# Kernel optimization log

Hardware: AMD Instinct MI355X
Metric: run time of the kernel (lower is better)

## Reference

```python
import jax, jax.numpy as jnp
import numpy as np

N = 100000      # nodes
E = 1600000     # edges (avg degree 16)
D = 64          # in_dim == hidden_dim
L = 4           # layer_gin
G = 128         # graphs in batch
BN_EPS = 1e-5


def setup_inputs() -> dict:
    key = jax.random.key(0)
    ks = jax.random.split(key, 9)
    x = jax.random.normal(ks[0], (N, D), dtype=jnp.float32)
    edge_index = jax.random.randint(ks[1], (2, E), 0, N, dtype=jnp.int32)
    batch = jnp.sort(jax.random.randint(ks[2], (N,), 0, G, dtype=jnp.int32))
    s = 0.05
    W1 = jax.random.normal(ks[3], (L, D, D), dtype=jnp.float32) * s
    b1 = jax.random.normal(ks[4], (L, D), dtype=jnp.float32) * s
    gamma = jnp.ones((L, D), dtype=jnp.float32)
    beta = jnp.zeros((L, D), dtype=jnp.float32)
    W2 = jax.random.normal(ks[5], (L, D, D), dtype=jnp.float32) * s
    b2 = jax.random.normal(ks[6], (L, D), dtype=jnp.float32) * s
    return dict(x=x, edge_index=edge_index, batch=batch,
                W1=W1, b1=b1, gamma=gamma, beta=beta, W2=W2, b2=b2)


def reference(x, edge_index, batch, W1, b1, gamma, beta, W2, b2):
    n = x.shape[0]
    src, dst = edge_index[0], edge_index[1]  # flow source_to_target
    # in-degree for mean aggregation (clamped to avoid div-by-zero)
    deg = jax.ops.segment_sum(jnp.ones(src.shape, x.dtype), dst, num_segments=n)
    inv_deg = 1.0 / jnp.maximum(deg, 1.0)
    # graph sizes for global mean pool
    gcnt = jax.ops.segment_sum(jnp.ones((n,), x.dtype), batch, num_segments=G)
    inv_gcnt = 1.0 / jnp.maximum(gcnt, 1.0)

    h = x
    node_pool = jnp.zeros((n, W2.shape[-1]), x.dtype)
    g_pool = jnp.zeros((G, W2.shape[-1]), x.dtype)
    for l in range(L):  # small fixed layer count
        # scatter-mean neighbor aggregation: [E,D] gather -> segment_sum
        agg = jax.ops.segment_sum(h[src], dst, num_segments=n) * inv_deg[:, None]
        z = (h + agg) @ W1[l] + b1[l]          # eps=0: (1+eps)*x + mean_j x_j
        mu = z.mean(axis=0)
        var = z.var(axis=0)                     # biased, as torch BatchNorm1d
        z = (z - mu) * jax.lax.rsqrt(var + BN_EPS) * gamma[l] + beta[l]
        h = jax.nn.relu(z) @ W2[l] + b2[l]
        node_pool = node_pool + h
        g_pool = g_pool + jax.ops.segment_sum(h, batch, num_segments=G) * inv_gcnt[:, None]
    return node_pool, g_pool
```

## Files before the change

kernel.cpp:

```cpp
#include <hip/hip_runtime.h>

#define N_NODES 100000
#define N_EDGES 1600000
#define DIM 64
#define NLAYER 4
#define NGRAPH 128
#define BN_EPS 1e-5f
#define NSHARD 16
#define AGG_CHUNK 16
#define NCHUNK (N_NODES / AGG_CHUNK)

typedef unsigned short ushort_t;
typedef unsigned int uint_t;
typedef __attribute__((ext_vector_type(8))) short short8;
typedef __attribute__((ext_vector_type(4))) float f32x4;
typedef __attribute__((ext_vector_type(4))) uint_t uintx4;

__device__ __forceinline__ ushort_t f2bf(float f) {
    uint_t u = __float_as_uint(f);
    uint_t r = (u + 0x7FFFu + ((u >> 16) & 1u)) >> 16;
    return (ushort_t)r;
}
__device__ __forceinline__ float bf2f(ushort_t u) {
    return __uint_as_float((uint_t)u << 16);
}
__device__ __forceinline__ void bf8_to_f32(const uint4 v, float f[8]) {
    f[0] = __uint_as_float(v.x << 16);
    f[1] = __uint_as_float(v.x & 0xFFFF0000u);
    f[2] = __uint_as_float(v.y << 16);
    f[3] = __uint_as_float(v.y & 0xFFFF0000u);
    f[4] = __uint_as_float(v.z << 16);
    f[5] = __uint_as_float(v.z & 0xFFFF0000u);
    f[6] = __uint_as_float(v.w << 16);
    f[7] = __uint_as_float(v.w & 0xFFFF0000u);
}


__global__ void k_hist(const int* __restrict__ ei, int* __restrict__ cntS,
                       int* __restrict__ rank,
                       const float* __restrict__ x, ushort_t* __restrict__ xh) {
    int e = blockIdx.x * blockDim.x + threadIdx.x;
    if (e < N_EDGES) {
        const float4 v = ((const float4*)x)[e];
        int d = ei[N_EDGES + e];
        int s = blockIdx.x & (NSHARD - 1);
        rank[e] = atomicAdd(&cntS[s * N_NODES + d], 1);
        ushort4 u;
        u.x = f2bf(v.x); u.y = f2bf(v.y); u.z = f2bf(v.z); u.w = f2bf(v.w);
        ((ushort4*)xh)[e] = u;
    }
}

__global__ void k_sumscan(int* __restrict__ cntS, int* __restrict__ cnt,
                          int* __restrict__ exc, int* __restrict__ bsums) {
    __shared__ int s[256];
    int i = blockIdx.x * 256 + threadIdx.x;
    int run = 0;
    if (i < N_NODES) {
#pragma unroll
        for (int sh = 0; sh < NSHARD; sh++) {
            int c = cntS[sh * N_NODES + i];
            cntS[sh * N_NODES + i] = run;
            run += c;
        }
        cnt[i] = run;
    }
    s[threadIdx.x] = run;
    __syncthreads();
    for (int off = 1; off < 256; off <<= 1) {
        int t = (threadIdx.x >= off) ? s[threadIdx.x - off] : 0;
        __syncthreads();
        s[threadIdx.x] += t;
        __syncthreads();
    }
    if (i < N_NODES) exc[i] = s[threadIdx.x] - run;
    if (threadIdx.x == 255) bsums[blockIdx.x] = s[255];
}

__global__ void k_scan2(const int* __restrict__ bsums, int* __restrict__ boffs, int nb) {
    __shared__ int s[512];
    int v = ((int)threadIdx.x < nb) ? bsums[threadIdx.x] : 0;
    s[threadIdx.x] = v;
    __syncthreads();
    for (int off = 1; off < 512; off <<= 1) {
        int t = (threadIdx.x >= off) ? s[threadIdx.x - off] : 0;
        __syncthreads();
        s[threadIdx.x] += t;
        __syncthreads();
    }
    if ((int)threadIdx.x < nb) boffs[threadIdx.x] = s[threadIdx.x] - v;
}

__global__ void k_scan3(int* __restrict__ exc, const int* __restrict__ boffs,
                        const int* __restrict__ cnt, const int* __restrict__ batch,
                        float* __restrict__ invdeg, float* __restrict__ invg) {
    int i = blockIdx.x * 256 + threadIdx.x;
    if (i < N_NODES) {
        exc[i] += boffs[blockIdx.x];
        invdeg[i] = 1.0f / (float)max(cnt[i], 1);
    }
    if (i < NGRAPH) {
        int key = i, lo = 0, hi = N_NODES;
        while (lo < hi) { int m = (lo + hi) >> 1; if (batch[m] < key) lo = m + 1; else hi = m; }
        int a = lo;
        key = i + 1; lo = 0; hi = N_NODES;
        while (lo < hi) { int m = (lo + hi) >> 1; if (batch[m] < key) lo = m + 1; else hi = m; }
        invg[i] = 1.0f / (float)max(lo - a, 1);
    }
}

__global__ void k_fill(const int* __restrict__ ei, const int* __restrict__ rowptr,
                       const int* __restrict__ cntS, const int* __restrict__ rank,
                       int* __restrict__ csr) {
    int e = blockIdx.x * blockDim.x + threadIdx.x;
    if (e < N_EDGES) {
        int d = ei[N_EDGES + e];
        int s = blockIdx.x & (NSHARD - 1);
        csr[rowptr[d] + cntS[s * N_NODES + d] + rank[e]] = ei[e];
    }
}

__device__ __forceinline__ void grp8b(const ushort_t* __restrict__ h,
                                      const int* __restrict__ cp,
                                      int e, int deg, int q, int r,
                                      float acc[8]) {
    const int last = deg - 1;
    const int e0 = e + q;
    int i0 = cp[min(e0, last)];
    float m0 = (e0 < deg) ? 1.f : 0.f;
    const uint4 v = *(const uint4*)(h + (size_t)i0 * 64 + r * 8);
    float f[8];
    bf8_to_f32(v, f);
#pragma unroll
    for (int j = 0; j < 8; j++) acc[j] = fmaf(f[j], m0, acc[j]);
}


__global__ __launch_bounds__(256, 8)
void k_passA(const ushort_t* __restrict__ h, const float* __restrict__ W1,
             const float* __restrict__ b1,
             const int* __restrict__ rowptr, const int* __restrict__ cnt,
             const int* __restrict__ csr, const float* __restrict__ invdeg,
             ushort_t* __restrict__ tglob, float* __restrict__ colsum,
             float* __restrict__ colsumsq) {
    __shared__ ushort_t wfrag[512 * 8];
    __shared__ uint_t smt[4][16 * 36];
    __shared__ float red[128];

    const int w = threadIdx.x >> 6;
    const int lane = threadIdx.x & 63;
    const int q = lane >> 3;
    const int r = lane & 7;
    const int wid = __builtin_amdgcn_readfirstlane((blockIdx.x << 2) | w);
    const bool active = wid < NCHUNK;
    const int n0 = (active ? wid : 0) * AGG_CHUNK;

    for (int s = threadIdx.x; s < 512; s += 256) {
        const int hh = s >> 8, c = (s >> 6) & 3, L = s & 63;
        const int kb = hh * 32 + ((L >> 4) * 8);
        const int out = c * 16 + (L & 15);
        uint_t* dst = (uint_t*)&wfrag[s * 8];
#pragma unroll
        for (int j2 = 0; j2 < 4; j2++) {
            const float lo = W1[(kb + 2 * j2) * 64 + out];
            const float hi = W1[(kb + 2 * j2 + 1) * 64 + out];
            dst[j2] = (uint_t)f2bf(lo) | ((uint_t)f2bf(hi) << 16);
        }
    }
    if (threadIdx.x < 128) red[threadIdx.x] = 0.f;
    __syncthreads();

    if (active) {
        for (int pp = 0; pp < AGG_CHUNK; pp += 2) {
            const int n = n0 + pp;
            const int sa = rowptr[n],     da = cnt[n];
            const int sb = rowptr[n + 1], db = cnt[n + 1];
            const float idga = invdeg[n], idgb = invdeg[n + 1];
            const int* __restrict__ ca = csr + sa;
            const int* __restrict__ cb = csr + sb;

            float aa[8] = {0,0,0,0,0,0,0,0};
            float ab[8] = {0,0,0,0,0,0,0,0};
            const int mm = min(da, db);
            int e = 0;
            for (; e < mm; e += 8) {
                grp8b(h, ca, e, da, q, r, aa);
                grp8b(h, cb, e, db, q, r, ab);
            }
            for (; e < da; e += 8) grp8b(h, ca, e, da, q, r, aa);
            for (; e < db; e += 8) grp8b(h, cb, e, db, q, r, ab);

#pragma unroll
            for (int j = 0; j < 8; j++) {
                aa[j] += __shfl_xor(aa[j], 8, 64);
                aa[j] += __shfl_xor(aa[j], 16, 64);
                aa[j] += __shfl_xor(aa[j], 32, 64);
                ab[j] += __shfl_xor(ab[j], 8, 64);
                ab[j] += __shfl_xor(ab[j], 16, 64);
                ab[j] += __shfl_xor(ab[j], 32, 64);
            }

            const uint4 sva = *(const uint4*)(h + (size_t)n * 64 + r * 8);
            const uint4 svb = *(const uint4*)(h + (size_t)(n + 1) * 64 + r * 8);
            float sa8[8], sb8[8];
            bf8_to_f32(sva, sa8);
            bf8_to_f32(svb, sb8);
            float ta[8], tb[8];
#pragma unroll
            for (int j = 0; j < 8; j++) {
                ta[j] = fmaf(aa[j], idga, sa8[j]);
                tb[j] = fmaf(ab[j], idgb, sb8[j]);
            }

            if (q < 2) {
                const int row = pp + q;
                uint_t* dst = &smt[w][row * 36 + r * 4];
#pragma unroll
                for (int j2 = 0; j2 < 4; j2++) {
                    const float lo = q ? tb[2 * j2]     : ta[2 * j2];
                    const float hi = q ? tb[2 * j2 + 1] : ta[2 * j2 + 1];
                    dst[j2] = (uint_t)f2bf(lo) | ((uint_t)f2bf(hi) << 16);
                }
            }
        }
    }

    if (active) {
        const int rr = lane >> 2, c4 = lane & 3;
        const uint_t* src = &smt[w][rr * 36 + c4 * 8];
        uintx4 v0, v1;
#pragma unroll
        for (int j = 0; j < 4; j++) { v0[j] = src[j]; v1[j] = src[4 + j]; }
        uintx4* dst = (uintx4*)((uint_t*)tglob + (size_t)(n0 + rr) * 32) + c4 * 2;
        __builtin_nontemporal_store(v0, dst);
        __builtin_nontemporal_store(v1, dst + 1);
    }

    const int m = lane & 15;
    const int quad = lane >> 4;
    const short8 a0 = *(const short8*)&smt[w][m * 36 + quad * 4];
    const short8 a1 = *(const short8*)&smt[w][m * 36 + 16 + quad * 4];

    float lsum[4], lsq[4];
#pragma unroll
    for (int c = 0; c < 4; c++) {
        const short8 b0 = *(const short8*)&wfrag[(size_t)(c * 64 + lane) * 8];
        const short8 b1f = *(const short8*)&wfrag[(size_t)((4 + c) * 64 + lane) * 8];
        f32x4 D = {0.f, 0.f, 0.f, 0.f};
        D = __builtin_amdgcn_mfma_f32_16x16x32_bf16(a0, b0, D, 0, 0, 0);
        D = __builtin_amdgcn_mfma_f32_16x16x32_bf16(a1, b1f, D, 0, 0, 0);
        const float bv = b1[c * 16 + m];
        float s = 0.f, sq = 0.f;
#pragma unroll
        for (int reg = 0; reg < 4; reg++) {
            const float zv = D[reg] + bv;
            s += zv;
            sq += zv * zv;
        }
        lsum[c] = s;
        lsq[c] = sq;
    }

    if (active) {
#pragma unroll
        for (int c = 0; c < 4; c++) {
            float s = lsum[c], sq = lsq[c];
            s += __shfl_xor(s, 16, 64);
            s += __shfl_xor(s, 32, 64);
            sq += __shfl_xor(sq, 16, 64);
            sq += __shfl_xor(sq, 32, 64);
            if (quad == 0) {
                atomicAdd(&red[c * 16 + m], s);
                atomicAdd(&red[64 + c * 16 + m], sq);
            }
        }
    }
    __syncthreads();
    if (threadIdx.x < 64) {
        atomicAdd(&colsum[threadIdx.x], red[threadIdx.x]);
        atomicAdd(&colsumsq[threadIdx.x], red[64 + threadIdx.x]);
    }
}


__global__ __launch_bounds__(256, 4)
void k_passB(const ushort_t* __restrict__ t, const float* __restrict__ W1,
             const float* __restrict__ b1, const float* __restrict__ W2,
             const float* __restrict__ b2, const float* __restrict__ colsum,
             const float* __restrict__ colsumsq, const float* __restrict__ gamma,
             const float* __restrict__ beta, ushort_t* __restrict__ hout) {
    __shared__ ushort_t wf1[512 * 8];
    __shared__ ushort_t wf2[512 * 8];
    __shared__ float sscale[64], sshift[64];
    __shared__ float ltile[4][16 * 68];

    const int w = threadIdx.x >> 6;
    const int lane = threadIdx.x & 63;
    const int wid = __builtin_amdgcn_readfirstlane((blockIdx.x << 2) | w);
    const bool active = wid < NCHUNK;
    const int n0 = (active ? wid : 0) * AGG_CHUNK;

    for (int s = threadIdx.x; s < 1024; s += 256) {
        const int which = s >> 9, t2 = s & 511;
        const int hh = t2 >> 8, c = (t2 >> 6) & 3, L = t2 & 63;
        const int kb = hh * 32 + ((L >> 4) * 8);
        const int out = c * 16 + (L & 15);
        const float* W = which ? W2 : W1;
        uint_t* dst = (uint_t*)&(which ? wf2 : wf1)[t2 * 8];
#pragma unroll
        for (int j2 = 0; j2 < 4; j2++) {
            const float lo = W[(kb + 2 * j2) * 64 + out];
            const float hi = W[(kb + 2 * j2 + 1) * 64 + out];
            dst[j2] = (uint_t)f2bf(lo) | ((uint_t)f2bf(hi) << 16);
        }
    }
    if (threadIdx.x < 64) {
        const float invn = 1.0f / (float)N_NODES;
        const float mu = colsum[threadIdx.x] * invn;
        const float var = colsumsq[threadIdx.x] * invn - mu * mu;
        const float sc = gamma[threadIdx.x] * rsqrtf(var + BN_EPS);
        sscale[threadIdx.x] = sc;
        sshift[threadIdx.x] = beta[threadIdx.x] - mu * sc;
    }
    __syncthreads();

    const int m = lane & 15;
    const int quad = lane >> 4;

    const ushort_t* tp = t + (size_t)(n0 + m) * 64;
    const short8 a0 = __builtin_nontemporal_load((const short8*)(tp + quad * 8));
    const short8 a1 = __builtin_nontemporal_load((const short8*)(tp + 32 + quad * 8));

#pragma unroll
    for (int c = 0; c < 4; c++) {
        const short8 b0 = *(const short8*)&wf1[(size_t)(c * 64 + lane) * 8];
        const short8 b1f = *(const short8*)&wf1[(size_t)((4 + c) * 64 + lane) * 8];
        f32x4 D = {0.f, 0.f, 0.f, 0.f};
        D = __builtin_amdgcn_mfma_f32_16x16x32_bf16(a0, b0, D, 0, 0, 0);
        D = __builtin_amdgcn_mfma_f32_16x16x32_bf16(a1, b1f, D, 0, 0, 0);
        const int col = c * 16 + m;
        const float bv = b1[col];
        const float sc = sscale[col], sh = sshift[col];
#pragma unroll
        for (int reg = 0; reg < 4; reg++) {
            const float zv = D[reg] + bv;
            ltile[w][(quad * 4 + reg) * 68 + col] = fmaxf(fmaf(zv, sc, sh), 0.f);
        }
    }

    const float* lr = &ltile[w][m * 68];
    float r0[8], r1[8];
#pragma unroll
    for (int j = 0; j < 8; j++) {
        r0[j] = lr[quad * 8 + j];
        r1[j] = lr[32 + quad * 8 + j];
    }
    union { uint_t u[4]; short8 v; } pa0, pa1;
#pragma unroll
    for (int j2 = 0; j2 < 4; j2++) {
        pa0.u[j2] = (uint_t)f2bf(r0[2 * j2]) | ((uint_t)f2bf(r0[2 * j2 + 1]) << 16);
        pa1.u[j2] = (uint_t)f2bf(r1[2 * j2]) | ((uint_t)f2bf(r1[2 * j2 + 1]) << 16);
    }
    const short8 c0 = pa0.v;
    const short8 c1 = pa1.v;

#pragma unroll
    for (int c = 0; c < 4; c++) {
        const short8 b0 = *(const short8*)&wf2[(size_t)(c * 64 + lane) * 8];
        const short8 b1f = *(const short8*)&wf2[(size_t)((4 + c) * 64 + lane) * 8];
        f32x4 D = {0.f, 0.f, 0.f, 0.f};
        D = __builtin_amdgcn_mfma_f32_16x16x32_bf16(c0, b0, D, 0, 0, 0);
        D = __builtin_amdgcn_mfma_f32_16x16x32_bf16(c1, b1f, D, 0, 0, 0);
        const float bv = b2[c * 16 + m];
#pragma unroll
        for (int reg = 0; reg < 4; reg++)
            ltile[w][(quad * 4 + reg) * 68 + c * 16 + m] = D[reg] + bv;
    }

    if (active) {
#pragma unroll
        for (int n = 0; n < 16; n++) {
            const float hv = ltile[w][n * 68 + lane];
            hout[(size_t)(n0 + n) * 64 + lane] = f2bf(hv);
        }
    }
}


#define POOL_CHUNK 64

__global__ void k_pool(const ushort_t* __restrict__ h1, const ushort_t* __restrict__ h2,
                       const ushort_t* __restrict__ h3, const ushort_t* __restrict__ h4,
                       const int* __restrict__ batch, float* __restrict__ node_pool,
                       float* __restrict__ gacc) {
    const int lane = threadIdx.x & 63;
    const int wid = (blockIdx.x << 2) | (threadIdx.x >> 6);
    const int n0 = wid * POOL_CHUNK;
    if (n0 >= N_NODES) return;
    const int n1 = min(N_NODES, n0 + POOL_CHUNK);
    int curg = -1;
    float ga = 0.f;
    for (int n = n0; n < n1; n++) {
        const size_t off = (size_t)n * 64 + lane;
        const float v = bf2f(h1[off]) + bf2f(h2[off]) + bf2f(h3[off]) + bf2f(h4[off]);
        __builtin_nontemporal_store(v, &node_pool[off]);
        const int g = batch[n];
        if (g != curg) {
            if (curg >= 0) atomicAdd(&gacc[curg * 64 + lane], ga);
            ga = 0.f;
            curg = g;
        }
        ga += v;
    }
    if (curg >= 0) atomicAdd(&gacc[curg * 64 + lane], ga);
}

__global__ void k_gfinal(const float* __restrict__ gacc, const float* __restrict__ invg,
                         float* __restrict__ gout) {
    int i = blockIdx.x * blockDim.x + threadIdx.x;
    if (i < NGRAPH * 64) gout[i] = gacc[i] * invg[i >> 6];
}


extern "C" void kernel_launch(void* const* d_in, const int* in_sizes, int n_in,
                              void* d_out, int out_size, void* d_ws, size_t ws_size,
                              hipStream_t stream) {
    (void)in_sizes; (void)n_in; (void)out_size; (void)ws_size;
    const float* x     = (const float*)d_in[0];
    const int*   ei    = (const int*)d_in[1];
    const int*   batch = (const int*)d_in[2];
    const float* W1    = (const float*)d_in[3];
    const float* b1    = (const float*)d_in[4];
    const float* gamma = (const float*)d_in[5];
    const float* beta  = (const float*)d_in[6];
    const float* W2    = (const float*)d_in[7];
    const float* b2    = (const float*)d_in[8];
    float* out = (float*)d_out;

    size_t o = 0;
    size_t o_cntS    = o; o += (size_t)NSHARD * N_NODES;
    size_t o_colsum  = o; o += (size_t)NLAYER * 64;
    size_t o_colsq   = o; o += (size_t)NLAYER * 64;
    size_t o_gacc    = o; o += (size_t)NGRAPH * 64;
    size_t zero_elems = o;
    size_t o_cnt     = o; o += N_NODES;
    size_t o_rowptr  = o; o += N_NODES;
    size_t o_bsums   = o; o += 512;
    size_t o_boffs   = o; o += 512;
    size_t o_invdeg  = o; o += N_NODES;
    size_t o_invg    = o; o += NGRAPH;
    size_t o_rank    = o; o += N_EDGES;
    size_t o_csr     = o; o += N_EDGES;
    size_t o_t       = o; o += (size_t)N_NODES * 32;
    size_t o_h0      = o; o += (size_t)N_NODES * 32;
    size_t o_h1      = o; o += (size_t)N_NODES * 32;
    size_t o_h2      = o; o += (size_t)N_NODES * 32;
    size_t o_xh      = o; o += (size_t)N_NODES * 32;

    int*   wsi = (int*)d_ws;
    float* wsf = (float*)d_ws;
    int*      cntS   = wsi + o_cntS;
    float*    colsum = wsf + o_colsum;
    float*    colsq  = wsf + o_colsq;
    float*    gacc   = wsf + o_gacc;
    int*      cnt    = wsi + o_cnt;
    int*      rowptr = wsi + o_rowptr;
    int*      bsums  = wsi + o_bsums;
    int*      boffs  = wsi + o_boffs;
    float*    invdeg = wsf + o_invdeg;
    float*    invg   = wsf + o_invg;
    int*      rank   = wsi + o_rank;
    int*      csr    = wsi + o_csr;
    ushort_t* tbuf   = (ushort_t*)(wsi + o_t);
    ushort_t* hb0    = (ushort_t*)(wsi + o_h0);
    ushort_t* hb1    = (ushort_t*)(wsi + o_h1);
    ushort_t* hb2    = (ushort_t*)(wsi + o_h2);
    ushort_t* xh     = (ushort_t*)(wsi + o_xh);

    hipMemsetAsync(d_ws, 0, zero_elems * 4, stream);

    const int eb = (N_EDGES + 255) / 256;
    const int nb = (N_NODES + 255) / 256;

    k_hist<<<eb, 256, 0, stream>>>(ei, cntS, rank, x, xh);
    k_sumscan<<<nb, 256, 0, stream>>>(cntS, cnt, rowptr, bsums);
    k_scan2<<<1, 512, 0, stream>>>(bsums, boffs, nb);
    k_scan3<<<nb, 256, 0, stream>>>(rowptr, boffs, cnt, batch, invdeg, invg);
    k_fill<<<eb, 256, 0, stream>>>(ei, rowptr, cntS, rank, csr);

    const ushort_t* hin[NLAYER]  = {xh,  hb0, hb1, hb2};
    ushort_t*       hoz[NLAYER]  = {hb0, hb1, hb2, xh};

    const int gridA = (NCHUNK + 3) / 4;
    for (int l = 0; l < NLAYER; l++) {
        k_passA<<<gridA, 256, 0, stream>>>(hin[l], W1 + l * 4096, b1 + l * 64,
                                           rowptr, cnt, csr, invdeg,
                                           tbuf, colsum + l * 64, colsq + l * 64);
        k_passB<<<gridA, 256, 0, stream>>>(tbuf, W1 + l * 4096, b1 + l * 64,
                                           W2 + l * 4096, b2 + l * 64,
                                           colsum + l * 64, colsq + l * 64,
                                           gamma + l * 64, beta + l * 64, hoz[l]);
    }
    const int gridP = (N_NODES + POOL_CHUNK * 4 - 1) / (POOL_CHUNK * 4);
    k_pool<<<gridP, 256, 0, stream>>>(hb0, hb1, hb2, xh, batch, out, gacc);
    k_gfinal<<<32, 256, 0, stream>>>(gacc, invg, out + (size_t)N_NODES * 64);
}
```

Baseline: 566.6 us.

## Fuse pooling into last passB and drop the per-edge rank buffer in CSR build

The final layer's passB now sums its output tile with the three previous layer outputs, writes node_pool directly and accumulates graph pools, so the separate pool kernel and the bf16 write and reread of the last layer are gone. The CSR build also stops storing a per-edge rank array: fill takes its slot with a second atomicAdd on the scanned shard counters. This removes the 1.6M-entry rank write and read, but fill now performs atomics. Edge order within a CSR row becomes nondeterministic, which can change the floating-point summation order.

```diff
diff --git a/kernel.cpp b/kernel.cpp
--- a/kernel.cpp
+++ b/kernel.cpp
@@ -37,14 +37,13 @@
 
 
 __global__ void k_hist(const int* __restrict__ ei, int* __restrict__ cntS,
-                       int* __restrict__ rank,
                        const float* __restrict__ x, ushort_t* __restrict__ xh) {
     int e = blockIdx.x * blockDim.x + threadIdx.x;
     if (e < N_EDGES) {
         const float4 v = ((const float4*)x)[e];
         int d = ei[N_EDGES + e];
         int s = blockIdx.x & (NSHARD - 1);
-        rank[e] = atomicAdd(&cntS[s * N_NODES + d], 1);
+        atomicAdd(&cntS[s * N_NODES + d], 1);
         ushort4 u;
         u.x = f2bf(v.x); u.y = f2bf(v.y); u.z = f2bf(v.z); u.w = f2bf(v.w);
         ((ushort4*)xh)[e] = u;
@@ -110,13 +109,13 @@
 }
 
 __global__ void k_fill(const int* __restrict__ ei, const int* __restrict__ rowptr,
-                       const int* __restrict__ cntS, const int* __restrict__ rank,
-                       int* __restrict__ csr) {
+                       int* __restrict__ cntS, int* __restrict__ csr) {
     int e = blockIdx.x * blockDim.x + threadIdx.x;
     if (e < N_EDGES) {
         int d = ei[N_EDGES + e];
         int s = blockIdx.x & (NSHARD - 1);
-        csr[rowptr[d] + cntS[s * N_NODES + d] + rank[e]] = ei[e];
+        int ofs = atomicAdd(&cntS[s * N_NODES + d], 1);
+        csr[rowptr[d] + ofs] = ei[e];
     }
 }
 
@@ -288,7 +287,10 @@
              const float* __restrict__ b1, const float* __restrict__ W2,
              const float* __restrict__ b2, const float* __restrict__ colsum,
              const float* __restrict__ colsumsq, const float* __restrict__ gamma,
-             const float* __restrict__ beta, ushort_t* __restrict__ hout) {
+             const float* __restrict__ beta, ushort_t* __restrict__ hout,
+             const ushort_t* __restrict__ ph0, const ushort_t* __restrict__ ph1,
+             const ushort_t* __restrict__ ph2, const int* __restrict__ batch,
+             float* __restrict__ node_pool, float* __restrict__ gacc, int last) {
     __shared__ ushort_t wf1[512 * 8];
     __shared__ ushort_t wf2[512 * 8];
     __shared__ float sscale[64], sshift[64];
@@ -378,41 +380,32 @@
     }
 
     if (active) {
-#pragma unroll
-        for (int n = 0; n < 16; n++) {
-            const float hv = ltile[w][n * 68 + lane];
-            hout[(size_t)(n0 + n) * 64 + lane] = f2bf(hv);
-        }
-    }
-}
-
-
-#define POOL_CHUNK 64
-
-__global__ void k_pool(const ushort_t* __restrict__ h1, const ushort_t* __restrict__ h2,
-                       const ushort_t* __restrict__ h3, const ushort_t* __restrict__ h4,
-                       const int* __restrict__ batch, float* __restrict__ node_pool,
-                       float* __restrict__ gacc) {
-    const int lane = threadIdx.x & 63;
-    const int wid = (blockIdx.x << 2) | (threadIdx.x >> 6);
-    const int n0 = wid * POOL_CHUNK;
-    if (n0 >= N_NODES) return;
-    const int n1 = min(N_NODES, n0 + POOL_CHUNK);
-    int curg = -1;
-    float ga = 0.f;
-    for (int n = n0; n < n1; n++) {
-        const size_t off = (size_t)n * 64 + lane;
-        const float v = bf2f(h1[off]) + bf2f(h2[off]) + bf2f(h3[off]) + bf2f(h4[off]);
-        __builtin_nontemporal_store(v, &node_pool[off]);
-        const int g = batch[n];
-        if (g != curg) {
+        if (last) {
+            int curg = -1;
+            float ga = 0.f;
+#pragma unroll 4
+            for (int n = 0; n < 16; n++) {
+                const size_t off = (size_t)(n0 + n) * 64 + lane;
+                const float v = ltile[w][n * 68 + lane] +
+                                bf2f(ph0[off]) + bf2f(ph1[off]) + bf2f(ph2[off]);
+                __builtin_nontemporal_store(v, &node_pool[off]);
+                const int g = batch[n0 + n];
+                if (g != curg) {
+                    if (curg >= 0) atomicAdd(&gacc[curg * 64 + lane], ga);
+                    ga = 0.f;
+                    curg = g;
+                }
+                ga += v;
+            }
             if (curg >= 0) atomicAdd(&gacc[curg * 64 + lane], ga);
-            ga = 0.f;
-            curg = g;
-        }
-        ga += v;
-    }
-    if (curg >= 0) atomicAdd(&gacc[curg * 64 + lane], ga);
+        } else {
+#pragma unroll
+            for (int n = 0; n < 16; n++) {
+                const float hv = ltile[w][n * 68 + lane];
+                hout[(size_t)(n0 + n) * 64 + lane] = f2bf(hv);
+            }
+        }
+    }
 }
 
 __global__ void k_gfinal(const float* __restrict__ gacc, const float* __restrict__ invg,
@@ -449,7 +442,6 @@
     size_t o_boffs   = o; o += 512;
     size_t o_invdeg  = o; o += N_NODES;
     size_t o_invg    = o; o += NGRAPH;
-    size_t o_rank    = o; o += N_EDGES;
     size_t o_csr     = o; o += N_EDGES;
     size_t o_t       = o; o += (size_t)N_NODES * 32;
     size_t o_h0      = o; o += (size_t)N_NODES * 32;
@@ -469,7 +461,6 @@
     int*      boffs  = wsi + o_boffs;
     float*    invdeg = wsf + o_invdeg;
     float*    invg   = wsf + o_invg;
-    int*      rank   = wsi + o_rank;
     int*      csr    = wsi + o_csr;
     ushort_t* tbuf   = (ushort_t*)(wsi + o_t);
     ushort_t* hb0    = (ushort_t*)(wsi + o_h0);
@@ -482,14 +473,14 @@
     const int eb = (N_EDGES + 255) / 256;
     const int nb = (N_NODES + 255) / 256;
 
-    k_hist<<<eb, 256, 0, stream>>>(ei, cntS, rank, x, xh);
+    k_hist<<<eb, 256, 0, stream>>>(ei, cntS, x, xh);
     k_sumscan<<<nb, 256, 0, stream>>>(cntS, cnt, rowptr, bsums);
     k_scan2<<<1, 512, 0, stream>>>(bsums, boffs, nb);
     k_scan3<<<nb, 256, 0, stream>>>(rowptr, boffs, cnt, batch, invdeg, invg);
-    k_fill<<<eb, 256, 0, stream>>>(ei, rowptr, cntS, rank, csr);
+    k_fill<<<eb, 256, 0, stream>>>(ei, rowptr, cntS, csr);
 
     const ushort_t* hin[NLAYER]  = {xh,  hb0, hb1, hb2};
-    ushort_t*       hoz[NLAYER]  = {hb0, hb1, hb2, xh};
+    ushort_t*       hoz[NLAYER]  = {hb0, hb1, hb2, nullptr};
 
     const int gridA = (NCHUNK + 3) / 4;
     for (int l = 0; l < NLAYER; l++) {
@@ -499,9 +490,9 @@
         k_passB<<<gridA, 256, 0, stream>>>(tbuf, W1 + l * 4096, b1 + l * 64,
                                            W2 + l * 4096, b2 + l * 64,
                                            colsum + l * 64, colsq + l * 64,
-                                           gamma + l * 64, beta + l * 64, hoz[l]);
-    }
-    const int gridP = (N_NODES + POOL_CHUNK * 4 - 1) / (POOL_CHUNK * 4);
-    k_pool<<<gridP, 256, 0, stream>>>(hb0, hb1, hb2, xh, batch, out, gacc);
+                                           gamma + l * 64, beta + l * 64, hoz[l],
+                                           hb0, hb1, hb2, batch, out, gacc,
+                                           (l == NLAYER - 1) ? 1 : 0);
+    }
     k_gfinal<<<32, 256, 0, stream>>>(gacc, invg, out + (size_t)N_NODES * 64);
 }
```

After: 592.6 us. 1.05x slower.
